# Kernel tuning notes

Measured on AMD Instinct MI355X. Metric: run time of the kernel, lower is better.

The kernel has to match this reference:

```python
import jax, jax.numpy as jnp
import numpy as np

HEAD_DIM = 64
R = 4            # region_token_num
THETA = 10000.0


def _rope_cos_sin(pos, D, theta):
    # pos: [B, L] int -> cos/sin [B, 1, L, D] (half-split / GPT-NeoX layout)
    inv_freq = theta ** (-(jnp.arange(0, D, 2, dtype=jnp.float32) / D))  # [D/2]
    ang = pos.astype(jnp.float32)[..., None] * inv_freq                  # [B, L, D/2]
    cos = jnp.concatenate([jnp.cos(ang), jnp.cos(ang)], axis=-1)[:, None]
    sin = jnp.concatenate([jnp.sin(ang), jnp.sin(ang)], axis=-1)[:, None]
    return cos, sin


def _apply_rope(x, cos, sin):
    # x: [B, H, L, D]
    D = x.shape[-1]
    x1, x2 = x[..., : D // 2], x[..., D // 2 :]
    rot = jnp.concatenate([-x2, x1], axis=-1)
    return x * cos + rot * sin


def _local_positions(regions):
    # index within contiguous region run: [B, T]
    B, T = regions.shape
    idx = jnp.arange(T, dtype=jnp.int32)
    is_new = jnp.concatenate(
        [jnp.ones((B, 1), bool), regions[:, 1:] != regions[:, :-1]], axis=1
    )
    start = jax.lax.cummax(jnp.where(is_new, idx[None, :], 0), axis=1)
    return idx[None, :] - start


def reference(query_q, x_k, x_v, regions, t_mask, n_mask, max_n):
    B, H, P, D = query_q.shape
    T = regions.shape[1]

    # ---- local RoPE positions: pool tokens all 0 (use_pool_offset=False),
    # x tokens: local index within region + R, zeroed on pads
    pool_pos = jnp.zeros((B, P), dtype=jnp.int32)
    x_pos = (_local_positions(regions) + R) * (regions > 0).astype(jnp.int32)

    cq, sq = _rope_cos_sin(pool_pos, D, THETA)
    ck, sk = _rope_cos_sin(x_pos, D, THETA)
    q = _apply_rope(query_q, cq, sq)
    k = _apply_rope(x_k, ck, sk)

    # ---- block-diagonal (same-region) cross-attention mask [B, 1, P, T]
    pool_region = jnp.repeat(jnp.arange(1, max_n + 1, dtype=regions.dtype), R)  # [P]
    pool_valid = jnp.repeat(n_mask, R, axis=1)                                   # [B, P]
    same = pool_region[None, :, None] == regions[:, None, :]
    valid = pool_valid[:, :, None] & t_mask[:, None, :]
    non_pad = (pool_region != 0)[None, :, None] & (regions != 0)[:, None, :]
    mask = (same & valid & non_pad)[:, None]                                     # [B,1,P,T]

    # ---- SDPA
    scale = 1.0 / jnp.sqrt(jnp.asarray(D, jnp.float32))
    scores = jnp.einsum('bhpd,bhtd->bhpt', q, k) * scale
    scores = jnp.where(mask, scores, jnp.asarray(-1e30, scores.dtype))
    attn = jax.nn.softmax(scores, axis=-1)
    return jnp.einsum('bhpt,bhtd->bhpd', attn, x_v)


def setup_inputs() -> dict:
    key = jax.random.key(0)
    k1, k2, k3, k4 = jax.random.split(key, 4)
    B, H, T, max_n = 4, 16, 4096, 64
    P = max_n * R
    regions = jnp.sort(jax.random.randint(k4, (B, T), 0, 65), axis=1)
    return {
        'query_q': jax.random.normal(k1, (B, H, P, HEAD_DIM), jnp.float32),
        'x_k': jax.random.normal(k2, (B, H, T, HEAD_DIM), jnp.float32),
        'x_v': jax.random.normal(k3, (B, H, T, HEAD_DIM), jnp.float32),
        'regions': regions,
        't_mask': jnp.ones((B, T), dtype=bool),
        'n_mask': jnp.ones((B, max_n), dtype=bool),
        'max_n': max_n,
    }
```

## Files before the change

kernel.cpp:

```cpp
#include <hip/hip_runtime.h>
#include <math.h>

#define NB   4
#define NH   16
#define NT   4096
#define ND   64
#define NP   256
#define NREG 64
#define RPOS 4

#define INVF_LOG2 0.4152410118609203f
#define QSCALE 0.18033688011112042f

__global__ void seg_kernel(const int* __restrict__ regions, int* __restrict__ bound) {
    const int b = blockIdx.x;
    const int* rb = regions + b * NT;
    int* bb = bound + b * 66;
    if (threadIdx.x < 66) bb[threadIdx.x] = NT;
    __syncthreads();
    for (int i = threadIdx.x; i < NT; i += blockDim.x) {
        const int r  = rb[i];
        const int rp = (i == 0) ? -1 : rb[i - 1];
        for (int v = rp + 1; v <= r; ++v) bb[v] = i;
    }
}

__global__ __launch_bounds__(256) void lca_kernel(
    const float* __restrict__ q,
    const float* __restrict__ k,
    const float* __restrict__ v,
    const int*   __restrict__ bound,
    float*       __restrict__ out)
{
    const int tid  = threadIdx.x;
    const int wave = tid >> 6;
    const int lane = tid & 63;
    const int grp  = lane >> 3;
    const int li   = lane & 7;
    const int dlo  = li << 2;

    const int blk = blockIdx.x;
    const int rg  = blk & 15;
    const int h   = (blk >> 4) & (NH - 1);
    const int b   = blk >> 8;
    const int ri  = (rg << 2) + wave;
    const int p0  = ri << 2;

    const size_t bh = (size_t)(b * NH + h);
    const float* kb = k + bh * (size_t)(NT * ND);
    const float* vb = v + bh * (size_t)(NT * ND);
    const float* qb = q + (bh * NP + p0) * ND;

    float qs[4][8];
    #pragma unroll
    for (int p = 0; p < 4; ++p) {
        const float4 qa = *(const float4*)(qb + p * ND + dlo);
        const float4 qc = *(const float4*)(qb + p * ND + 32 + dlo);
        qs[p][0] = qa.x * QSCALE; qs[p][1] = qa.y * QSCALE;
        qs[p][2] = qa.z * QSCALE; qs[p][3] = qa.w * QSCALE;
        qs[p][4] = qc.x * QSCALE; qs[p][5] = qc.y * QSCALE;
        qs[p][6] = qc.z * QSCALE; qs[p][7] = qc.w * QSCALE;
    }

    const int s   = bound[b * 66 + ri + 1];
    const int e   = bound[b * 66 + ri + 2];
    const int cnt = e - s;

    float l4[4] = {0.f, 0.f, 0.f, 0.f};
    float acc[4][8];
    #pragma unroll
    for (int p = 0; p < 4; ++p)
        #pragma unroll
        for (int i = 0; i < 8; ++i) acc[p][i] = 0.f;

    if (cnt > 0) {
        float frq[4];
        #pragma unroll
        for (int i = 0; i < 4; ++i)
            frq[i] = exp2f(-INVF_LOG2 * (float)(dlo + i));

        const int iters = (cnt + 7) >> 3;

        const int tA = min(s + grp, e - 1);
        const int tB = min(s + 8 + grp, e - 1);
        const float* pA = kb + (size_t)tA * ND;
        const float* pB = kb + (size_t)tB * ND;
        const float* qA = vb + (size_t)tA * ND;
        const float* qB = vb + (size_t)tB * ND;
        float4 kc0 = *(const float4*)(pA + dlo);
        float4 kc1 = *(const float4*)(pA + 32 + dlo);
        float4 vc0 = *(const float4*)(qA + dlo);
        float4 vc1 = *(const float4*)(qA + 32 + dlo);
        float4 kn0 = *(const float4*)(pB + dlo);
        float4 kn1 = *(const float4*)(pB + 32 + dlo);
        float4 vn0 = *(const float4*)(qB + dlo);
        float4 vn1 = *(const float4*)(qB + 32 + dlo);

        #pragma unroll 2
        for (int it = 0; it < iters; ++it) {
            const int tp = min(s + ((it + 2) << 3) + grp, e - 1);
            const float* kp = kb + (size_t)tp * ND;
            const float* vp = vb + (size_t)tp * ND;
            const float4 kp0 = *(const float4*)(kp + dlo);
            const float4 kp1 = *(const float4*)(kp + 32 + dlo);
            const float4 vp0 = *(const float4*)(vp + dlo);
            const float4 vp1 = *(const float4*)(vp + 32 + dlo);

            const int   off   = (it << 3) + grp;
            const bool  valid = off < cnt;
            const float pos   = (float)(off + RPOS);

            const float klo[4] = {kc0.x, kc0.y, kc0.z, kc0.w};
            const float khi[4] = {kc1.x, kc1.y, kc1.z, kc1.w};
            float pd0 = 0.f, pd1 = 0.f, pd2 = 0.f, pd3 = 0.f;
            #pragma unroll
            for (int i = 0; i < 4; ++i) {
                float sa, ca;
                __sincosf(pos * frq[i], &sa, &ca);
                const float rlo = klo[i] * ca - khi[i] * sa;
                const float rhi = khi[i] * ca + klo[i] * sa;
                pd0 = fmaf(rlo, qs[0][i], fmaf(rhi, qs[0][i + 4], pd0));
                pd1 = fmaf(rlo, qs[1][i], fmaf(rhi, qs[1][i + 4], pd1));
                pd2 = fmaf(rlo, qs[2][i], fmaf(rhi, qs[2][i + 4], pd2));
                pd3 = fmaf(rlo, qs[3][i], fmaf(rhi, qs[3][i + 4], pd3));
            }
            #pragma unroll
            for (int m = 1; m <= 4; m <<= 1) {
                pd0 += __shfl_xor(pd0, m);
                pd1 += __shfl_xor(pd1, m);
                pd2 += __shfl_xor(pd2, m);
                pd3 += __shfl_xor(pd3, m);
            }
            const float w0 = valid ? exp2f(pd0) : 0.f;
            const float w1 = valid ? exp2f(pd1) : 0.f;
            const float w2 = valid ? exp2f(pd2) : 0.f;
            const float w3 = valid ? exp2f(pd3) : 0.f;
            l4[0] += w0; l4[1] += w1; l4[2] += w2; l4[3] += w3;
            const float vx[8] = {vc0.x, vc0.y, vc0.z, vc0.w, vc1.x, vc1.y, vc1.z, vc1.w};
            #pragma unroll
            for (int i = 0; i < 8; ++i) {
                acc[0][i] = fmaf(w0, vx[i], acc[0][i]);
                acc[1][i] = fmaf(w1, vx[i], acc[1][i]);
                acc[2][i] = fmaf(w2, vx[i], acc[2][i]);
                acc[3][i] = fmaf(w3, vx[i], acc[3][i]);
            }
            kc0 = kn0; kc1 = kn1; vc0 = vn0; vc1 = vn1;
            kn0 = kp0; kn1 = kp1; vn0 = vp0; vn1 = vp1;
        }
    } else {
        for (int t = grp; t < NT; t += 8) {
            const float* vp = vb + (size_t)t * ND;
            const float4 va = *(const float4*)(vp + dlo);
            const float4 vc = *(const float4*)(vp + 32 + dlo);
            acc[0][0] += va.x; acc[0][1] += va.y; acc[0][2] += va.z; acc[0][3] += va.w;
            acc[0][4] += vc.x; acc[0][5] += vc.y; acc[0][6] += vc.z; acc[0][7] += vc.w;
        }
        #pragma unroll
        for (int p = 1; p < 4; ++p)
            #pragma unroll
            for (int i = 0; i < 8; ++i) acc[p][i] = acc[0][i];
        l4[0] = l4[1] = l4[2] = l4[3] = (float)NT * 0.125f;
    }

    #pragma unroll
    for (int m = 8; m <= 32; m <<= 1) {
        #pragma unroll
        for (int p = 0; p < 4; ++p) {
            l4[p] += __shfl_xor(l4[p], m);
            #pragma unroll
            for (int i = 0; i < 8; ++i) acc[p][i] += __shfl_xor(acc[p][i], m);
        }
    }

    #pragma unroll
    for (int p = 0; p < 4; ++p) {
        if (grp == p) {
            const float inv = 1.f / l4[p];
            float* op = out + (bh * NP + p0 + p) * ND;
            *(float4*)(op + dlo) = make_float4(acc[p][0] * inv, acc[p][1] * inv,
                                               acc[p][2] * inv, acc[p][3] * inv);
            *(float4*)(op + 32 + dlo) = make_float4(acc[p][4] * inv, acc[p][5] * inv,
                                                    acc[p][6] * inv, acc[p][7] * inv);
        }
    }
}

extern "C" void kernel_launch(void* const* d_in, const int* in_sizes, int n_in,
                              void* d_out, int out_size, void* d_ws, size_t ws_size,
                              hipStream_t stream) {
    (void)in_sizes; (void)n_in; (void)ws_size; (void)out_size;
    const float* q       = (const float*)d_in[0];
    const float* k       = (const float*)d_in[1];
    const float* v       = (const float*)d_in[2];
    const int*   regions = (const int*)d_in[3];
    float* out   = (float*)d_out;
    int*   bound = (int*)d_ws;

    seg_kernel<<<dim3(NB), 1024, 0, stream>>>(regions, bound);
    lca_kernel<<<dim3(NB * NH * (NREG / 4)), 256, 0, stream>>>(q, k, v, bound, out);
}
```

Before: 34.91 us.

## Fuse region-boundary search into attention kernel via wave ballot search

After: 30.40 us. -12.9%, faster.

```diff
diff --git a/kernel.cpp b/kernel.cpp
--- a/kernel.cpp
+++ b/kernel.cpp
@@ -12,24 +12,13 @@
 #define INVF_LOG2 0.4152410118609203f
 #define QSCALE 0.18033688011112042f
 
-__global__ void seg_kernel(const int* __restrict__ regions, int* __restrict__ bound) {
-    const int b = blockIdx.x;
-    const int* rb = regions + b * NT;
-    int* bb = bound + b * 66;
-    if (threadIdx.x < 66) bb[threadIdx.x] = NT;
-    __syncthreads();
-    for (int i = threadIdx.x; i < NT; i += blockDim.x) {
-        const int r  = rb[i];
-        const int rp = (i == 0) ? -1 : rb[i - 1];
-        for (int v = rp + 1; v <= r; ++v) bb[v] = i;
-    }
-}
+typedef float vfloat4 __attribute__((ext_vector_type(4)));
 
 __global__ __launch_bounds__(256) void lca_kernel(
     const float* __restrict__ q,
     const float* __restrict__ k,
     const float* __restrict__ v,
-    const int*   __restrict__ bound,
+    const int*   __restrict__ regions,
     float*       __restrict__ out)
 {
     const int tid  = threadIdx.x;
@@ -50,6 +39,9 @@
     const float* kb = k + bh * (size_t)(NT * ND);
     const float* vb = v + bh * (size_t)(NT * ND);
     const float* qb = q + (bh * NP + p0) * ND;
+    const int*   rb = regions + b * NT;
+
+    const int samp = rb[lane << 6];
 
     float qs[4][8];
     #pragma unroll
@@ -62,8 +54,16 @@
         qs[p][6] = qc.z * QSCALE; qs[p][7] = qc.w * QSCALE;
     }
 
-    const int s   = bound[b * 66 + ri + 1];
-    const int e   = bound[b * 66 + ri + 2];
+    const int c1  = __popcll(__ballot(samp < ri + 1));
+    const int c2  = __popcll(__ballot(samp < ri + 2));
+    const int st1 = (c1 == 0) ? 0 : ((c1 - 1) << 6) + 1;
+    const int st2 = (c2 == 0) ? 0 : ((c2 - 1) << 6) + 1;
+    const int i1  = st1 + lane;
+    const int i2  = st2 + lane;
+    const int w1  = (i1 < NT) ? rb[i1] : 0x7fffffff;
+    const int w2  = (i2 < NT) ? rb[i2] : 0x7fffffff;
+    const int s   = st1 + __popcll(__ballot(w1 < ri + 1));
+    const int e   = st2 + __popcll(__ballot(w2 < ri + 2));
     const int cnt = e - s;
 
     float l4[4] = {0.f, 0.f, 0.f, 0.f};
@@ -132,17 +132,17 @@
                 pd3 += __shfl_xor(pd3, m);
             }
             const float w0 = valid ? exp2f(pd0) : 0.f;
-            const float w1 = valid ? exp2f(pd1) : 0.f;
-            const float w2 = valid ? exp2f(pd2) : 0.f;
-            const float w3 = valid ? exp2f(pd3) : 0.f;
-            l4[0] += w0; l4[1] += w1; l4[2] += w2; l4[3] += w3;
+            const float w1v = valid ? exp2f(pd1) : 0.f;
+            const float w2v = valid ? exp2f(pd2) : 0.f;
+            const float w3v = valid ? exp2f(pd3) : 0.f;
+            l4[0] += w0; l4[1] += w1v; l4[2] += w2v; l4[3] += w3v;
             const float vx[8] = {vc0.x, vc0.y, vc0.z, vc0.w, vc1.x, vc1.y, vc1.z, vc1.w};
             #pragma unroll
             for (int i = 0; i < 8; ++i) {
-                acc[0][i] = fmaf(w0, vx[i], acc[0][i]);
-                acc[1][i] = fmaf(w1, vx[i], acc[1][i]);
-                acc[2][i] = fmaf(w2, vx[i], acc[2][i]);
-                acc[3][i] = fmaf(w3, vx[i], acc[3][i]);
+                acc[0][i] = fmaf(w0,  vx[i], acc[0][i]);
+                acc[1][i] = fmaf(w1v, vx[i], acc[1][i]);
+                acc[2][i] = fmaf(w2v, vx[i], acc[2][i]);
+                acc[3][i] = fmaf(w3v, vx[i], acc[3][i]);
             }
             kc0 = kn0; kc1 = kn1; vc0 = vn0; vc1 = vn1;
             kn0 = kp0; kn1 = kp1; vn0 = vp0; vn1 = vp1;
@@ -177,10 +177,12 @@
         if (grp == p) {
             const float inv = 1.f / l4[p];
             float* op = out + (bh * NP + p0 + p) * ND;
-            *(float4*)(op + dlo) = make_float4(acc[p][0] * inv, acc[p][1] * inv,
-                                               acc[p][2] * inv, acc[p][3] * inv);
-            *(float4*)(op + 32 + dlo) = make_float4(acc[p][4] * inv, acc[p][5] * inv,
-                                                    acc[p][6] * inv, acc[p][7] * inv);
+            const vfloat4 o0 = {acc[p][0] * inv, acc[p][1] * inv,
+                                acc[p][2] * inv, acc[p][3] * inv};
+            const vfloat4 o1 = {acc[p][4] * inv, acc[p][5] * inv,
+                                acc[p][6] * inv, acc[p][7] * inv};
+            __builtin_nontemporal_store(o0, (vfloat4*)(op + dlo));
+            __builtin_nontemporal_store(o1, (vfloat4*)(op + 32 + dlo));
         }
     }
 }
@@ -188,14 +190,12 @@
 extern "C" void kernel_launch(void* const* d_in, const int* in_sizes, int n_in,
                               void* d_out, int out_size, void* d_ws, size_t ws_size,
                               hipStream_t stream) {
-    (void)in_sizes; (void)n_in; (void)ws_size; (void)out_size;
+    (void)in_sizes; (void)n_in; (void)d_ws; (void)ws_size; (void)out_size;
     const float* q       = (const float*)d_in[0];
     const float* k       = (const float*)d_in[1];
     const float* v       = (const float*)d_in[2];
     const int*   regions = (const int*)d_in[3];
-    float* out   = (float*)d_out;
-    int*   bound = (int*)d_ws;
-
-    seg_kernel<<<dim3(NB), 1024, 0, stream>>>(regions, bound);
-    lca_kernel<<<dim3(NB * NH * (NREG / 4)), 256, 0, stream>>>(q, k, v, bound, out);
+    float* out = (float*)d_out;
+
+    lca_kernel<<<dim3(NB * NH * (NREG / 4)), 256, 0, stream>>>(q, k, v, regions, out);
 }
```
